# Kernel optimization log

Measured on AMD Instinct MI355X. Metric: run time of the kernel, lower is better.

Reference implementation:

```python
import jax, jax.numpy as jnp
import numpy as np

INPUT, HIDDEN, OUTPUT = 512, 1024, 512
B, T = 64, 512

def setup_inputs() -> dict:
    key = jax.random.key(0)
    k1, k2, k3, k4 = jax.random.split(key, 4)
    s_xh = (2.0 / (INPUT + HIDDEN)) ** 0.5
    s_hy = (2.0 / (INPUT + OUTPUT)) ** 0.5
    return {
        "x": jax.random.normal(k1, (B, T, INPUT), dtype=jnp.float32),
        "W_xh": jax.random.normal(k2, (INPUT, HIDDEN), dtype=jnp.float32) * s_xh,
        "W_hh": jax.random.normal(k3, (HIDDEN, HIDDEN), dtype=jnp.float32) * s_xh,
        "b_h": jnp.zeros((HIDDEN,), dtype=jnp.float32),
        "W_hy": jax.random.normal(k4, (HIDDEN, OUTPUT), dtype=jnp.float32) * s_hy,
        "b_y": jnp.zeros((OUTPUT,), dtype=jnp.float32),
    }

def reference(x, W_xh, W_hh, b_h, W_hy, b_y):
    Bn, Tn, _ = x.shape
    # precompute input projection for all timesteps: [B, T, H]
    xW = jnp.einsum("bti,ih->bth", x, W_xh)
    h0 = jnp.zeros((Bn, W_hh.shape[0]), dtype=x.dtype)

    def step(h, xw_t):  # xw_t: [B, H]
        h = jnp.tanh(h @ W_hh + xw_t + b_h)
        y = h @ W_hy + b_y  # [B, O]
        return h, y

    _, ys = jax.lax.scan(step, h0, jnp.swapaxes(xW, 0, 1))  # ys: [T, B, O]
    return jnp.swapaxes(ys, 0, 1)  # [B, T, O]
```

## Files before the change

kernel.cpp:

```cpp
#include <hip/hip_runtime.h>
#include <stdint.h>

#define B_  64
#define T_  512
#define IN_ 512
#define H_  1024
#define O_  512

typedef short  short8 __attribute__((ext_vector_type(8)));
typedef float  f32x4  __attribute__((ext_vector_type(4)));
typedef unsigned int uint32;

__device__ __forceinline__ unsigned short f2bf(float f) {
  uint32 u = __builtin_bit_cast(uint32, f);
  uint32 r = u + 0x7fffu + ((u >> 16) & 1u);
  return (unsigned short)(r >> 16);
}
__device__ __forceinline__ float bf2f(unsigned short h) {
  uint32 u = ((uint32)h) << 16;
  return __builtin_bit_cast(float, u);
}

__device__ __forceinline__ f32x4 mfma_bf16(short8 a, short8 b, f32x4 c) {
  return __builtin_amdgcn_mfma_f32_16x16x32_bf16(a, b, c, 0, 0, 0);
}

__device__ __forceinline__ short8 aload16(const unsigned short* p) {
  struct U { unsigned long long a, b; } u;
  u.a = __hip_atomic_load((const unsigned long long*)p,
                          __ATOMIC_RELAXED, __HIP_MEMORY_SCOPE_AGENT);
  u.b = __hip_atomic_load((const unsigned long long*)(p + 4),
                          __ATOMIC_RELAXED, __HIP_MEMORY_SCOPE_AGENT);
  return __builtin_bit_cast(short8, u);
}

__global__ __launch_bounds__(256) void g1_xh(
    const float* __restrict__ x, const float* __restrict__ Wxh,
    const float* __restrict__ bh, unsigned short* __restrict__ xwH)
{
  const int blk = blockIdx.x;
  const int mt = blk >> 4;
  const int nt = blk & 15;
  const int m0 = mt * 64, n0 = nt * 64;
  const int tid = threadIdx.x;
  const int wave = tid >> 6, lane = tid & 63;
  const int l15 = lane & 15, l4 = lane >> 4;

  __shared__ unsigned short sAhi[64 * 40];
  __shared__ unsigned short sAlo[64 * 40];
  __shared__ unsigned short sB[64 * 40];

  f32x4 acc[4] = { {0.f,0.f,0.f,0.f}, {0.f,0.f,0.f,0.f},
                   {0.f,0.f,0.f,0.f}, {0.f,0.f,0.f,0.f} };

  for (int kk = 0; kk < IN_ / 32; ++kk) {
    const int k0 = kk * 32;
#pragma unroll
    for (int q = 0; q < 2; ++q) {
      const int v = tid + q * 256;
      const int row = v >> 3;
      const int c4 = (v & 7) * 4;
      const float4 av = *(const float4*)(x + (size_t)(m0 + row) * IN_ + k0 + c4);
      unsigned short h0 = f2bf(av.x), h1 = f2bf(av.y), h2 = f2bf(av.z), h3 = f2bf(av.w);
      unsigned short g0 = f2bf(av.x - bf2f(h0)), g1 = f2bf(av.y - bf2f(h1));
      unsigned short g2 = f2bf(av.z - bf2f(h2)), g3 = f2bf(av.w - bf2f(h3));
      uint32* dh = (uint32*)&sAhi[row * 40 + c4];
      dh[0] = (uint32)h0 | ((uint32)h1 << 16);
      dh[1] = (uint32)h2 | ((uint32)h3 << 16);
      uint32* dl = (uint32*)&sAlo[row * 40 + c4];
      dl[0] = (uint32)g0 | ((uint32)g1 << 16);
      dl[1] = (uint32)g2 | ((uint32)g3 << 16);
    }
#pragma unroll
    for (int q = 0; q < 2; ++q) {
      const int v = tid + q * 256;
      const int k = v >> 4;
      const int n4 = (v & 15) * 4;
      const float4 bv = *(const float4*)(Wxh + (size_t)(k0 + k) * H_ + n0 + n4);
      sB[(n4 + 0) * 40 + k] = f2bf(bv.x);
      sB[(n4 + 1) * 40 + k] = f2bf(bv.y);
      sB[(n4 + 2) * 40 + k] = f2bf(bv.z);
      sB[(n4 + 3) * 40 + k] = f2bf(bv.w);
    }
    __syncthreads();
    const int arow = wave * 16 + l15;
    const short8 ahi = *(const short8*)&sAhi[arow * 40 + l4 * 8];
    const short8 alo = *(const short8*)&sAlo[arow * 40 + l4 * 8];
#pragma unroll
    for (int ct = 0; ct < 4; ++ct) {
      const short8 bf = *(const short8*)&sB[(ct * 16 + l15) * 40 + l4 * 8];
      acc[ct] = mfma_bf16(ahi, bf, acc[ct]);
      acc[ct] = mfma_bf16(alo, bf, acc[ct]);
    }
    __syncthreads();
  }
#pragma unroll
  for (int ct = 0; ct < 4; ++ct) {
    const int n = n0 + ct * 16 + l15;
    const float bias = bh[n];
#pragma unroll
    for (int i = 0; i < 4; ++i) {
      const int m = m0 + wave * 16 + l4 * 4 + i;
      xwH[(size_t)m * H_ + n] = f2bf(acc[ct][i] + bias);
    }
  }
}

#define GCn 32
#define NB  16
#define NC  32

__global__ __launch_bounds__(256) void rnn_rec(
    const float* __restrict__ Whh,
    unsigned short* __restrict__ xwH,
    unsigned short* __restrict__ rotlo,
    int* __restrict__ ctrl)
{
  const int blk = blockIdx.x;
  const int gb = blk >> 5;
  const int gc = blk & 31;
  const int rb0 = gb * NB;
  const int c0 = gc * NC;
  const int tid = threadIdx.x;
  const int wave = tid >> 6, lane = tid & 63;
  const int l15 = lane & 15, l4 = lane >> 4;
  const int kp0 = wave * 256;

  __shared__ __align__(16) float red[4][NB][NC];

  short8 Wf[8][2];
#pragma unroll
  for (int ks = 0; ks < 8; ++ks) {
#pragma unroll
    for (int ct = 0; ct < 2; ++ct) {
      const int n = c0 + ct * 16 + l15;
#pragma unroll
      for (int j = 0; j < 8; ++j) {
        const int k = kp0 + ks * 32 + l4 * 8 + j;
        Wf[ks][ct][j] = (short)f2bf(Whh[(size_t)k * H_ + n]);
      }
    }
  }

  int* cnt = ctrl + gb * 64;

  const int er = tid >> 4;
  const int p2 = (tid & 15) * 2;

  for (int t = 0; t < T_; ++t) {
    const size_t aXW = ((size_t)((rb0 + er) * T_ + t)) * H_ + c0 + p2;
    const uint32 xwu = *(const uint32*)(xwH + aXW);

    f32x4 acc0 = {0.f,0.f,0.f,0.f}, acc1 = {0.f,0.f,0.f,0.f};
    if (t > 0) {
      const unsigned short* lsrc = rotlo + (size_t)((t - 1) & 1) * (B_ * H_);
      const int brow = rb0 + l15;
      short8 Ahi[8], Alo[8];
#pragma unroll
      for (int ks = 0; ks < 8; ++ks) {
        const int k = kp0 + ks * 32 + l4 * 8;
        Ahi[ks] = aload16(xwH + (size_t)(brow * T_ + (t - 1)) * H_ + k);
        Alo[ks] = aload16(lsrc + (size_t)brow * H_ + k);
      }
#pragma unroll
      for (int ks = 0; ks < 8; ++ks) {
        acc0 = mfma_bf16(Ahi[ks], Wf[ks][0], acc0);
        acc0 = mfma_bf16(Alo[ks], Wf[ks][0], acc0);
        acc1 = mfma_bf16(Ahi[ks], Wf[ks][1], acc1);
        acc1 = mfma_bf16(Alo[ks], Wf[ks][1], acc1);
      }
    }
#pragma unroll
    for (int i = 0; i < 4; ++i) {
      red[wave][l4 * 4 + i][l15]      = acc0[i];
      red[wave][l4 * 4 + i][16 + l15] = acc1[i];
    }
    __syncthreads();
    {
      float sa = 0.f, sb = 0.f;
#pragma unroll
      for (int w = 0; w < 4; ++w) {
        const float2 v = *(const float2*)&red[w][er][p2];
        sa += v.x; sb += v.y;
      }
      const float h0 = tanhf(sa + bf2f((unsigned short)(xwu & 0xffffu)));
      const float h1 = tanhf(sb + bf2f((unsigned short)(xwu >> 16)));
      const unsigned short hh0 = f2bf(h0), hh1 = f2bf(h1);
      const unsigned short hl0 = f2bf(h0 - bf2f(hh0));
      const unsigned short hl1 = f2bf(h1 - bf2f(hh1));
      const uint32 hi32 = (uint32)hh0 | ((uint32)hh1 << 16);
      const uint32 lo32 = (uint32)hl0 | ((uint32)hl1 << 16);
      __hip_atomic_store((uint32*)(xwH + aXW), hi32,
                         __ATOMIC_RELAXED, __HIP_MEMORY_SCOPE_AGENT);
      unsigned short* ldst = rotlo + (size_t)(t & 1) * (B_ * H_);
      __hip_atomic_store((uint32*)(ldst + (size_t)(rb0 + er) * H_ + c0 + p2), lo32,
                         __ATOMIC_RELAXED, __HIP_MEMORY_SCOPE_AGENT);
    }
    asm volatile("s_waitcnt vmcnt(0)" ::: "memory");
    __syncthreads();
    if (tid == 0) {
      __hip_atomic_fetch_add(cnt, 1, __ATOMIC_RELAXED, __HIP_MEMORY_SCOPE_AGENT);
      const int want = GCn * (t + 1);
      while (__hip_atomic_load(cnt, __ATOMIC_RELAXED, __HIP_MEMORY_SCOPE_AGENT) < want) {
        __builtin_amdgcn_s_sleep(2);
      }
    }
    __syncthreads();
  }
}

__global__ __launch_bounds__(256) void g3_hy(
    const unsigned short* __restrict__ Hm, const float* __restrict__ Why,
    const float* __restrict__ by, float* __restrict__ out)
{
  const int blk = blockIdx.x;
  const int mt = blk >> 3;
  const int nt = blk & 7;
  const int m0 = mt * 64, n0 = nt * 64;
  const int tid = threadIdx.x;
  const int wave = tid >> 6, lane = tid & 63;
  const int l15 = lane & 15, l4 = lane >> 4;

  __shared__ unsigned short sA[64 * 40];
  __shared__ unsigned short sB[64 * 40];

  f32x4 acc[4] = { {0.f,0.f,0.f,0.f}, {0.f,0.f,0.f,0.f},
                   {0.f,0.f,0.f,0.f}, {0.f,0.f,0.f,0.f} };

  for (int kk = 0; kk < H_ / 32; ++kk) {
    const int k0 = kk * 32;
    {
      const int row = tid >> 2;
      const int c8 = (tid & 3) * 8;
      const short8 v = *(const short8*)(Hm + (size_t)(m0 + row) * H_ + k0 + c8);
      *(short8*)&sA[row * 40 + c8] = v;
    }
#pragma unroll
    for (int q = 0; q < 2; ++q) {
      const int v = tid + q * 256;
      const int k = v >> 4;
      const int n4 = (v & 15) * 4;
      const float4 bv = *(const float4*)(Why + (size_t)(k0 + k) * O_ + n0 + n4);
      sB[(n4 + 0) * 40 + k] = f2bf(bv.x);
      sB[(n4 + 1) * 40 + k] = f2bf(bv.y);
      sB[(n4 + 2) * 40 + k] = f2bf(bv.z);
      sB[(n4 + 3) * 40 + k] = f2bf(bv.w);
    }
    __syncthreads();
    const short8 a = *(const short8*)&sA[(wave * 16 + l15) * 40 + l4 * 8];
#pragma unroll
    for (int ct = 0; ct < 4; ++ct) {
      const short8 bf = *(const short8*)&sB[(ct * 16 + l15) * 40 + l4 * 8];
      acc[ct] = mfma_bf16(a, bf, acc[ct]);
    }
    __syncthreads();
  }
#pragma unroll
  for (int ct = 0; ct < 4; ++ct) {
    const int n = n0 + ct * 16 + l15;
    const float bias = by[n];
#pragma unroll
    for (int i = 0; i < 4; ++i) {
      const int m = m0 + wave * 16 + l4 * 4 + i;
      out[(size_t)m * O_ + n] = acc[ct][i] + bias;
    }
  }
}

extern "C" void kernel_launch(void* const* d_in, const int* in_sizes, int n_in,
                              void* d_out, int out_size, void* d_ws, size_t ws_size,
                              hipStream_t stream) {
  const float* x   = (const float*)d_in[0];
  const float* Wxh = (const float*)d_in[1];
  const float* Whh = (const float*)d_in[2];
  const float* bh  = (const float*)d_in[3];
  const float* Why = (const float*)d_in[4];
  const float* by  = (const float*)d_in[5];
  float* out = (float*)d_out;

  unsigned short* xwH   = (unsigned short*)d_ws;
  unsigned short* rotlo = (unsigned short*)((char*)d_ws + 67108864);
  int*            ctrl  = (int*)((char*)d_ws + 67108864 + 262144);

  hipMemsetAsync(ctrl, 0, 1024, stream);
  g1_xh<<<8192, 256, 0, stream>>>(x, Wxh, bh, xwH);
  rnn_rec<<<128, 256, 0, stream>>>(Whh, xwH, rotlo, ctrl);
  g3_hy<<<4096, 256, 0, stream>>>(xwH, Why, by, out);
}
```

Before: 3.833 ms.

## Widen recurrent blocks to 64 columns and use per-block flag barrier

The persistent recurrent kernel now gives each block 64 hidden columns instead of 32, so 64 blocks run instead of 128 and each group of batch rows has 16 participants per timestep barrier instead of 32. The shared atomic counter barrier is replaced by per-block flag stores that wave 0 polls together with a wave-wide all-check. Each thread also handles 4 outputs with 64-bit stores. The trade-off is less parallelism for the per-step MFMA work and more register pressure (W fragments doubled), in exchange for lower barrier latency and less atomic contention.

```diff
diff --git a/kernel.cpp b/kernel.cpp
--- a/kernel.cpp
+++ b/kernel.cpp
@@ -10,6 +10,7 @@
 typedef short  short8 __attribute__((ext_vector_type(8)));
 typedef float  f32x4  __attribute__((ext_vector_type(4)));
 typedef unsigned int uint32;
+typedef unsigned long long u64;
 
 __device__ __forceinline__ unsigned short f2bf(float f) {
   uint32 u = __builtin_bit_cast(uint32, f);
@@ -26,11 +27,9 @@
 }
 
 __device__ __forceinline__ short8 aload16(const unsigned short* p) {
-  struct U { unsigned long long a, b; } u;
-  u.a = __hip_atomic_load((const unsigned long long*)p,
-                          __ATOMIC_RELAXED, __HIP_MEMORY_SCOPE_AGENT);
-  u.b = __hip_atomic_load((const unsigned long long*)(p + 4),
-                          __ATOMIC_RELAXED, __HIP_MEMORY_SCOPE_AGENT);
+  struct U { u64 a, b; } u;
+  u.a = __hip_atomic_load((const u64*)p, __ATOMIC_RELAXED, __HIP_MEMORY_SCOPE_AGENT);
+  u.b = __hip_atomic_load((const u64*)(p + 4), __ATOMIC_RELAXED, __HIP_MEMORY_SCOPE_AGENT);
   return __builtin_bit_cast(short8, u);
 }
 
@@ -106,19 +105,19 @@
   }
 }
 
-#define GCn 32
 #define NB  16
-#define NC  32
-
-__global__ __launch_bounds__(256) void rnn_rec(
+#define NC  64
+#define GCn 16
+
+__global__ __launch_bounds__(256, 1) void rnn_rec(
     const float* __restrict__ Whh,
     unsigned short* __restrict__ xwH,
     unsigned short* __restrict__ rotlo,
     int* __restrict__ ctrl)
 {
   const int blk = blockIdx.x;
-  const int gb = blk >> 5;
-  const int gc = blk & 31;
+  const int gb = blk >> 4;
+  const int gc = blk & 15;
   const int rb0 = gb * NB;
   const int c0 = gc * NC;
   const int tid = threadIdx.x;
@@ -128,11 +127,11 @@
 
   __shared__ __align__(16) float red[4][NB][NC];
 
-  short8 Wf[8][2];
+  short8 Wf[8][4];
 #pragma unroll
   for (int ks = 0; ks < 8; ++ks) {
 #pragma unroll
-    for (int ct = 0; ct < 2; ++ct) {
+    for (int ct = 0; ct < 4; ++ct) {
       const int n = c0 + ct * 16 + l15;
 #pragma unroll
       for (int j = 0; j < 8; ++j) {
@@ -142,16 +141,18 @@
     }
   }
 
-  int* cnt = ctrl + gb * 64;
+  int* gflags = ctrl + gb * (GCn * 16);
+  int* myflag = gflags + gc * 16;
 
   const int er = tid >> 4;
-  const int p2 = (tid & 15) * 2;
+  const int c4 = (tid & 15) * 4;
 
   for (int t = 0; t < T_; ++t) {
-    const size_t aXW = ((size_t)((rb0 + er) * T_ + t)) * H_ + c0 + p2;
-    const uint32 xwu = *(const uint32*)(xwH + aXW);
-
-    f32x4 acc0 = {0.f,0.f,0.f,0.f}, acc1 = {0.f,0.f,0.f,0.f};
+    const size_t aXW = ((size_t)((rb0 + er) * T_ + t)) * H_ + c0 + c4;
+    const u64 xwu = *(const u64*)(xwH + aXW);
+
+    f32x4 acc[4] = { {0.f,0.f,0.f,0.f}, {0.f,0.f,0.f,0.f},
+                     {0.f,0.f,0.f,0.f}, {0.f,0.f,0.f,0.f} };
     if (t > 0) {
       const unsigned short* lsrc = rotlo + (size_t)((t - 1) & 1) * (B_ * H_);
       const int brow = rb0 + l15;
@@ -164,46 +165,59 @@
       }
 #pragma unroll
       for (int ks = 0; ks < 8; ++ks) {
-        acc0 = mfma_bf16(Ahi[ks], Wf[ks][0], acc0);
-        acc0 = mfma_bf16(Alo[ks], Wf[ks][0], acc0);
-        acc1 = mfma_bf16(Ahi[ks], Wf[ks][1], acc1);
-        acc1 = mfma_bf16(Alo[ks], Wf[ks][1], acc1);
-      }
-    }
-#pragma unroll
-    for (int i = 0; i < 4; ++i) {
-      red[wave][l4 * 4 + i][l15]      = acc0[i];
-      red[wave][l4 * 4 + i][16 + l15] = acc1[i];
+#pragma unroll
+        for (int ct = 0; ct < 4; ++ct) {
+          acc[ct] = mfma_bf16(Ahi[ks], Wf[ks][ct], acc[ct]);
+          acc[ct] = mfma_bf16(Alo[ks], Wf[ks][ct], acc[ct]);
+        }
+      }
+    }
+#pragma unroll
+    for (int ct = 0; ct < 4; ++ct) {
+#pragma unroll
+      for (int i = 0; i < 4; ++i) {
+        red[wave][l4 * 4 + i][ct * 16 + l15] = acc[ct][i];
+      }
     }
     __syncthreads();
     {
-      float sa = 0.f, sb = 0.f;
+      float s[4] = {0.f, 0.f, 0.f, 0.f};
 #pragma unroll
       for (int w = 0; w < 4; ++w) {
-        const float2 v = *(const float2*)&red[w][er][p2];
-        sa += v.x; sb += v.y;
-      }
-      const float h0 = tanhf(sa + bf2f((unsigned short)(xwu & 0xffffu)));
-      const float h1 = tanhf(sb + bf2f((unsigned short)(xwu >> 16)));
-      const unsigned short hh0 = f2bf(h0), hh1 = f2bf(h1);
-      const unsigned short hl0 = f2bf(h0 - bf2f(hh0));
-      const unsigned short hl1 = f2bf(h1 - bf2f(hh1));
-      const uint32 hi32 = (uint32)hh0 | ((uint32)hh1 << 16);
-      const uint32 lo32 = (uint32)hl0 | ((uint32)hl1 << 16);
-      __hip_atomic_store((uint32*)(xwH + aXW), hi32,
+        const f32x4 v = *(const f32x4*)&red[w][er][c4];
+#pragma unroll
+        for (int j = 0; j < 4; ++j) s[j] += v[j];
+      }
+      u64 hi64 = 0, lo64 = 0;
+#pragma unroll
+      for (int j = 0; j < 4; ++j) {
+        const float xwj = bf2f((unsigned short)((xwu >> (16 * j)) & 0xffffu));
+        const float h = tanhf(s[j] + xwj);
+        const unsigned short hh = f2bf(h);
+        const unsigned short hl = f2bf(h - bf2f(hh));
+        hi64 |= ((u64)hh) << (16 * j);
+        lo64 |= ((u64)hl) << (16 * j);
+      }
+      __hip_atomic_store((u64*)(xwH + aXW), hi64,
                          __ATOMIC_RELAXED, __HIP_MEMORY_SCOPE_AGENT);
       unsigned short* ldst = rotlo + (size_t)(t & 1) * (B_ * H_);
-      __hip_atomic_store((uint32*)(ldst + (size_t)(rb0 + er) * H_ + c0 + p2), lo32,
+      __hip_atomic_store((u64*)(ldst + (size_t)(rb0 + er) * H_ + c0 + c4), lo64,
                          __ATOMIC_RELAXED, __HIP_MEMORY_SCOPE_AGENT);
     }
     asm volatile("s_waitcnt vmcnt(0)" ::: "memory");
     __syncthreads();
     if (tid == 0) {
-      __hip_atomic_fetch_add(cnt, 1, __ATOMIC_RELAXED, __HIP_MEMORY_SCOPE_AGENT);
-      const int want = GCn * (t + 1);
-      while (__hip_atomic_load(cnt, __ATOMIC_RELAXED, __HIP_MEMORY_SCOPE_AGENT) < want) {
-        __builtin_amdgcn_s_sleep(2);
-      }
+      __hip_atomic_store(myflag, t + 1, __ATOMIC_RELAXED, __HIP_MEMORY_SCOPE_AGENT);
+    }
+    if (wave == 0) {
+      const int want = t + 1;
+      const int* fp = gflags + (lane & 15) * 16;
+      int v;
+      do {
+        v = __hip_atomic_load(fp, __ATOMIC_RELAXED, __HIP_MEMORY_SCOPE_AGENT);
+        if (__all(v >= want)) break;
+        __builtin_amdgcn_s_sleep(1);
+      } while (true);
     }
     __syncthreads();
   }
@@ -282,8 +296,8 @@
   unsigned short* rotlo = (unsigned short*)((char*)d_ws + 67108864);
   int*            ctrl  = (int*)((char*)d_ws + 67108864 + 262144);
 
-  hipMemsetAsync(ctrl, 0, 1024, stream);
+  hipMemsetAsync(ctrl, 0, 4096, stream);
   g1_xh<<<8192, 256, 0, stream>>>(x, Wxh, bh, xwH);
-  rnn_rec<<<128, 256, 0, stream>>>(Whh, xwH, rotlo, ctrl);
+  rnn_rec<<<64, 256, 0, stream>>>(Whh, xwH, rotlo, ctrl);
   g3_hy<<<4096, 256, 0, stream>>>(xwH, Why, by, out);
 }
```

After: 3.545 ms. 1.08x faster.
